# Kernel optimization log

Hardware: AMD Instinct MI355X
Metric: run time of the kernel (lower is better)

The kernel has to match this reference:

```python
import jax, jax.numpy as jnp
import numpy as np

N = 100000        # nodes
E = 1600000       # edges (avg degree 16)
IN_C = 128
HID = 128
OUT_C = 18


def setup_inputs() -> dict:
    key = jax.random.key(0)
    k_x, k_e, k_w1, k_b1, k_w2, k_b2 = jax.random.split(key, 6)
    x = jax.random.normal(k_x, (N, IN_C), dtype=jnp.float32)
    edge_index = jax.random.randint(k_e, (2, E), 0, N, dtype=jnp.int64)
    # Glorot-ish init for linear weights, zero bias (PyG GCNConv defaults)
    W1 = jax.random.normal(k_w1, (IN_C, HID), dtype=jnp.float32) / np.sqrt(IN_C)
    b1 = jnp.zeros((HID,), dtype=jnp.float32)
    W2 = jax.random.normal(k_w2, (HID, OUT_C), dtype=jnp.float32) / np.sqrt(HID)
    b2 = jnp.zeros((OUT_C,), dtype=jnp.float32)
    return {"x": x, "edge_index": edge_index, "W1": W1, "b1": b1, "W2": W2, "b2": b2}


def _gcn_conv(x, src, dst, norm, W, b, n_nodes):
    # PyG GCNConv: linear transform, then normalized scatter-add aggregation
    h = x @ W                                   # [N, d_out]
    msg = h[src] * norm[:, None]                # gather + scale: [E+N, d_out]
    out = jax.ops.segment_sum(msg, dst, num_segments=n_nodes)
    return out + b


def reference(x, edge_index, W1, b1, W2, b2):
    src, dst = edge_index[0], edge_index[1]
    loop = jnp.arange(N, dtype=edge_index.dtype)
    src_f = jnp.concatenate([src, loop])        # add self-loops
    dst_f = jnp.concatenate([dst, loop])
    # symmetric normalization deg^-1/2[src] * deg^-1/2[dst] (with self-loops)
    deg = jax.ops.segment_sum(jnp.ones_like(dst_f, dtype=x.dtype), dst_f, num_segments=N)
    dinv = jnp.where(deg > 0, jax.lax.rsqrt(deg), 0.0)
    norm = dinv[src_f] * dinv[dst_f]            # [E+N]

    h = _gcn_conv(x, src_f, dst_f, norm, W1, b1, N)
    h = jax.nn.relu(h)
    # dropout is identity in eval mode (training=False)
    h = _gcn_conv(h, src_f, dst_f, norm, W2, b2, N)
    return jax.nn.log_softmax(h, axis=1)
```

## Files before the change

kernel.cpp:

```cpp
#include <hip/hip_runtime.h>
#include <math.h>

#define NN 100000
#define NE 1600000
#define CH  128
#define CO  18
#define NPB 256
#define NBUK ((NN + NPB - 1) / NPB)
#define EPB 4096
#define NBB ((NE + EPB - 1) / EPB)

typedef unsigned int uint;
typedef unsigned short ushort;
typedef float floatx4 __attribute__((ext_vector_type(4)));
typedef short short8 __attribute__((ext_vector_type(8)));
typedef ushort ushort4v __attribute__((ext_vector_type(4)));

__device__ __forceinline__ float bf_lo(uint u) { return __uint_as_float(u << 16); }
__device__ __forceinline__ float bf_hi(uint u) { return __uint_as_float(u & 0xFFFF0000u); }
__device__ __forceinline__ ushort f2bf(float f) {
    uint u = __float_as_uint(f);
    u += 0x7FFFu + ((u >> 16) & 1u);
    return (ushort)(u >> 16);
}
__device__ __forceinline__ uint pack_bf16(float a, float b) {
    return (uint)f2bf(a) | ((uint)f2bf(b) << 16);
}


__global__ __launch_bounds__(256) void k_bhist(const int* __restrict__ dst,
                                               int* __restrict__ bcnt) {
    __shared__ int h[NBUK];
    int tid = threadIdx.x;
    for (int i = tid; i < NBUK; i += 256) h[i] = 0;
    __syncthreads();
    int e0 = blockIdx.x * EPB;
#pragma unroll
    for (int i = 0; i < EPB / 256; ++i) {
        int e = e0 + i * 256 + tid;
        if (e < NE) atomicAdd(&h[dst[e] >> 8], 1);
    }
    __syncthreads();
    for (int i = tid; i < NBUK; i += 256)
        if (h[i]) atomicAdd(&bcnt[i], h[i]);
}

__global__ __launch_bounds__(512) void k_bscan(const int* __restrict__ bcnt,
                                               int* __restrict__ bbase,
                                               int* __restrict__ bcur) {
    __shared__ int s[512];
    int tid = threadIdx.x;
    int c = (tid < NBUK) ? bcnt[tid] : 0;
    s[tid] = c;
    __syncthreads();
    for (int off = 1; off < 512; off <<= 1) {
        int t = (tid >= off) ? s[tid - off] : 0;
        __syncthreads();
        s[tid] += t;
        __syncthreads();
    }
    if (tid < NBUK) {
        int ex = s[tid] - c;
        bbase[tid] = ex;
        bcur[tid] = ex;
    }
    if (tid == NBUK) bbase[NBUK] = NE;
}

__global__ __launch_bounds__(256) void k_bin(const int* __restrict__ src,
                                             const int* __restrict__ dst,
                                             int* __restrict__ bcur,
                                             uint* __restrict__ etmp) {
    __shared__ int h[NBUK];
    __shared__ int base[NBUK];
    int tid = threadIdx.x;
    for (int i = tid; i < NBUK; i += 256) h[i] = 0;
    __syncthreads();

    int e0 = blockIdx.x * EPB;
    int sv[EPB / 256], dv[EPB / 256];
#pragma unroll
    for (int i = 0; i < EPB / 256; ++i) {
        int e = e0 + i * 256 + tid;
        if (e < NE) {
            sv[i] = src[e];
            dv[i] = dst[e];
            atomicAdd(&h[dv[i] >> 8], 1);
        } else {
            dv[i] = -1;
        }
    }
    __syncthreads();
    for (int i = tid; i < NBUK; i += 256)
        base[i] = h[i] ? atomicAdd(&bcur[i], h[i]) : 0;
    __syncthreads();
    for (int i = tid; i < NBUK; i += 256) h[i] = 0;
    __syncthreads();
#pragma unroll
    for (int i = 0; i < EPB / 256; ++i) {
        if (dv[i] >= 0) {
            int b = dv[i] >> 8;
            int pos = base[b] + atomicAdd(&h[b], 1);
            etmp[pos] = ((uint)sv[i] << 8) | ((uint)dv[i] & 255u);
        }
    }
}

__global__ __launch_bounds__(256) void k_pass2(const int* __restrict__ bbase,
                                               const uint* __restrict__ etmp,
                                               int* __restrict__ row_start,
                                               float* __restrict__ dinv,
                                               int* __restrict__ csr_src) {
    __shared__ int hist[NPB];
    __shared__ int s[NPB];
    __shared__ int cur[NPB];
    int tid = threadIdx.x;
    int b = blockIdx.x;
    int e0 = bbase[b], e1 = bbase[b + 1];

    hist[tid] = 0;
    __syncthreads();
    for (int e = e0 + tid; e < e1; e += 256)
        atomicAdd(&hist[etmp[e] & 255u], 1);
    __syncthreads();

    int c = hist[tid];
    s[tid] = c;
    __syncthreads();
    for (int off = 1; off < 256; off <<= 1) {
        int t = (tid >= off) ? s[tid - off] : 0;
        __syncthreads();
        s[tid] += t;
        __syncthreads();
    }
    int pfx = s[tid] - c;
    s[tid] = pfx;
    cur[tid] = 0;

    int node = b * NPB + tid;
    if (node < NN) {
        row_start[node] = e0 + pfx;
        dinv[node] = rsqrtf((float)c + 1.0f);
    }
    if (b == NBUK - 1 && tid == 0) row_start[NN] = NE;
    __syncthreads();

    for (int e = e0 + tid; e < e1; e += 256) {
        uint r = etmp[e];
        int n = (int)(r & 255u);
        int p = e0 + s[n] + atomicAdd(&cur[n], 1);
        csr_src[p] = (int)(r >> 8);
    }
}


__global__ __launch_bounds__(256) void k_wprep(const float* __restrict__ W1,
                                               ushort* __restrict__ Wt) {
    int t = blockIdx.x * 256 + threadIdx.x;
    if (t < 128 * 128) {
        int k = t >> 7, n = t & 127;
        Wt[n * 128 + k] = f2bf(W1[t]);
    }
}


__global__ __launch_bounds__(256, 2) void k_gemm1(const float* __restrict__ x,
                                                  const uint* __restrict__ Wtg,
                                                  ushort* __restrict__ h1s) {
    __shared__ ushort As[128 * 128];
    __shared__ ushort Bs[128 * 128];
    int tid = threadIdx.x;
    int row0 = blockIdx.x * 128;

    for (int i = 0; i < 32; ++i) {
        int j = i * 256 + tid;
        int n = j >> 6, ku = j & 63;
        int uidx = (n * 64 + ku) ^ ((n & 7) << 2);
        ((uint*)Bs)[uidx] = Wtg[j];
    }
    for (int i = 0; i < 16; ++i) {
        int flat = i * 256 + tid;
        int r = flat >> 5, c4 = flat & 31;
        int gr = row0 + r;
        float4 v = (gr < NN) ? ((const float4*)x)[(size_t)gr * 32 + c4]
                             : make_float4(0.f, 0.f, 0.f, 0.f);
        ushort4v p;
        p.x = f2bf(v.x); p.y = f2bf(v.y); p.z = f2bf(v.z); p.w = f2bf(v.w);
        int idx = (r * 128 + c4 * 4) ^ ((r & 7) << 3);
        *(ushort4v*)&As[idx] = p;
    }
    __syncthreads();

    int lane = tid & 63;
    int wave = tid >> 6;
    int wrow = wave * 32;
    int lr = lane & 15;
    int lk8 = (lane >> 4) * 8;

    floatx4 acc[2][8];
#pragma unroll
    for (int a = 0; a < 2; ++a)
#pragma unroll
        for (int b = 0; b < 8; ++b) acc[a][b] = (floatx4)(0.0f);

#pragma unroll
    for (int ks = 0; ks < 4; ++ks) {
        int k0 = ks * 32 + lk8;
        int r0r = wrow + lr;
        int r1r = wrow + 16 + lr;
        short8 a0 = *(const short8*)&As[(r0r * 128 + k0) ^ ((r0r & 7) << 3)];
        short8 a1 = *(const short8*)&As[(r1r * 128 + k0) ^ ((r1r & 7) << 3)];
#pragma unroll
        for (int nt = 0; nt < 8; ++nt) {
            int n = nt * 16 + lr;
            short8 bf = *(const short8*)&Bs[(n * 128 + k0) ^ ((n & 7) << 3)];
            acc[0][nt] = __builtin_amdgcn_mfma_f32_16x16x32_bf16(a0, bf, acc[0][nt], 0, 0, 0);
            acc[1][nt] = __builtin_amdgcn_mfma_f32_16x16x32_bf16(a1, bf, acc[1][nt], 0, 0, 0);
        }
    }

    int drow = (lane >> 4) * 4;
#pragma unroll
    for (int rt = 0; rt < 2; ++rt) {
#pragma unroll
        for (int i = 0; i < 4; ++i) {
            int gr = row0 + wrow + rt * 16 + drow + i;
            if (gr < NN) {
                size_t base = (size_t)gr * 128;
#pragma unroll
                for (int nt = 0; nt < 8; ++nt)
                    h1s[base + nt * 16 + lr] = f2bf(acc[rt][nt][i]);
            }
        }
    }
}


__global__ __launch_bounds__(256) void k_agg1(const int* __restrict__ row_start,
                                              const int* __restrict__ csr_src,
                                              const float* __restrict__ dinv,
                                              const uint* __restrict__ h1u,
                                              const float* __restrict__ b1,
                                              uint* __restrict__ h1ru) {
    int wave = threadIdx.x >> 6;
    int lane = threadIdx.x & 63;
    int i = blockIdx.x * 4 + wave;
    if (i >= NN) return;
    int r0 = row_start[i], r1 = row_start[i + 1];
    float di = dinv[i];
    float ax = 0.0f, ay = 0.0f;

    int j = r0;
    for (; j + 7 < r1; j += 8) {
        int s0 = csr_src[j],     s1 = csr_src[j + 1];
        int s2 = csr_src[j + 2], s3 = csr_src[j + 3];
        int s4 = csr_src[j + 4], s5 = csr_src[j + 5];
        int s6 = csr_src[j + 6], s7 = csr_src[j + 7];
        float w0 = dinv[s0] * di, w1 = dinv[s1] * di;
        float w2 = dinv[s2] * di, w3 = dinv[s3] * di;
        float w4 = dinv[s4] * di, w5 = dinv[s5] * di;
        float w6 = dinv[s6] * di, w7 = dinv[s7] * di;
        uint u0 = h1u[(size_t)s0 * 64 + lane];
        uint u1 = h1u[(size_t)s1 * 64 + lane];
        uint u2 = h1u[(size_t)s2 * 64 + lane];
        uint u3 = h1u[(size_t)s3 * 64 + lane];
        uint u4 = h1u[(size_t)s4 * 64 + lane];
        uint u5 = h1u[(size_t)s5 * 64 + lane];
        uint u6 = h1u[(size_t)s6 * 64 + lane];
        uint u7 = h1u[(size_t)s7 * 64 + lane];
        ax += w0 * bf_lo(u0) + w1 * bf_lo(u1) + w2 * bf_lo(u2) + w3 * bf_lo(u3)
            + w4 * bf_lo(u4) + w5 * bf_lo(u5) + w6 * bf_lo(u6) + w7 * bf_lo(u7);
        ay += w0 * bf_hi(u0) + w1 * bf_hi(u1) + w2 * bf_hi(u2) + w3 * bf_hi(u3)
            + w4 * bf_hi(u4) + w5 * bf_hi(u5) + w6 * bf_hi(u6) + w7 * bf_hi(u7);
    }
    for (; j < r1; ++j) {
        int s0 = csr_src[j];
        float w0 = dinv[s0] * di;
        uint u0 = h1u[(size_t)s0 * 64 + lane];
        ax += w0 * bf_lo(u0);
        ay += w0 * bf_hi(u0);
    }

    uint us = h1u[(size_t)i * 64 + lane];
    float2 bb = ((const float2*)b1)[lane];
    float di2 = di * di;
    float ox = fmaxf(ax + di2 * bf_lo(us) + bb.x, 0.0f);
    float oy = fmaxf(ay + di2 * bf_hi(us) + bb.y, 0.0f);
    h1ru[(size_t)i * 64 + lane] = pack_bf16(ox, oy);
}


__global__ __launch_bounds__(256, 2) void k_gemm2(const uint* __restrict__ h1ru,
                                                  const float* __restrict__ W2,
                                                  ushort* __restrict__ h2b) {
    __shared__ float xs[128][129];
    __shared__ float Ws[128 * 18];
    int row0 = blockIdx.x * 128;
    int tid = threadIdx.x;

    for (int i = tid; i < 128 * 18; i += 256) Ws[i] = W2[i];
    for (int i = tid; i < 128 * 64; i += 256) {
        int r = i >> 6, c2 = i & 63;
        int gr = row0 + r;
        uint u = (gr < NN) ? h1ru[(size_t)gr * 64 + c2] : 0u;
        xs[r][2 * c2]     = bf_lo(u);
        xs[r][2 * c2 + 1] = bf_hi(u);
    }
    __syncthreads();

    int rl   = tid & 127;
    int half = tid >> 7;
    int j0   = half * 9;
    float acc[9];
#pragma unroll
    for (int j = 0; j < 9; ++j) acc[j] = 0.0f;

#pragma unroll 4
    for (int k = 0; k < 128; ++k) {
        float xv = xs[rl][k];
#pragma unroll
        for (int j = 0; j < 9; ++j)
            acc[j] += xv * Ws[k * 18 + j0 + j];
    }
    int gr = row0 + rl;
    if (gr < NN) {
#pragma unroll
        for (int j = 0; j < 9; ++j)
            h2b[(size_t)gr * 24 + j0 + j] = f2bf(acc[j]);
    }
}


__device__ __forceinline__ void acc_row(float* acc, float w,
                                        uint4 a, uint4 b, uint c) {
    acc[0]  += w * bf_lo(a.x); acc[1]  += w * bf_hi(a.x);
    acc[2]  += w * bf_lo(a.y); acc[3]  += w * bf_hi(a.y);
    acc[4]  += w * bf_lo(a.z); acc[5]  += w * bf_hi(a.z);
    acc[6]  += w * bf_lo(a.w); acc[7]  += w * bf_hi(a.w);
    acc[8]  += w * bf_lo(b.x); acc[9]  += w * bf_hi(b.x);
    acc[10] += w * bf_lo(b.y); acc[11] += w * bf_hi(b.y);
    acc[12] += w * bf_lo(b.z); acc[13] += w * bf_hi(b.z);
    acc[14] += w * bf_lo(b.w); acc[15] += w * bf_hi(b.w);
    acc[16] += w * bf_lo(c);   acc[17] += w * bf_hi(c);
}

__global__ __launch_bounds__(256) void k_agg2(const int* __restrict__ row_start,
                                              const int* __restrict__ csr_src,
                                              const float* __restrict__ dinv,
                                              const uint* __restrict__ h2u,
                                              const float* __restrict__ b2,
                                              float* __restrict__ out) {
    int i = blockIdx.x * 256 + threadIdx.x;
    if (i >= NN) return;
    int r0 = row_start[i], r1 = row_start[i + 1];
    float di = dinv[i];
    float acc[CO];
#pragma unroll
    for (int j = 0; j < CO; ++j) acc[j] = 0.0f;

    int e = r0;
    for (; e + 3 < r1; e += 4) {
        int s0 = csr_src[e],     s1 = csr_src[e + 1];
        int s2 = csr_src[e + 2], s3 = csr_src[e + 3];
        float w0 = dinv[s0] * di, w1 = dinv[s1] * di;
        float w2 = dinv[s2] * di, w3 = dinv[s3] * di;
        const uint4* p0 = (const uint4*)(h2u + (size_t)s0 * 12);
        const uint4* p1 = (const uint4*)(h2u + (size_t)s1 * 12);
        const uint4* p2 = (const uint4*)(h2u + (size_t)s2 * 12);
        const uint4* p3 = (const uint4*)(h2u + (size_t)s3 * 12);
        uint4 a0 = p0[0], b0 = p0[1]; uint c0 = ((const uint*)p0)[8];
        uint4 a1 = p1[0], b1v = p1[1]; uint c1 = ((const uint*)p1)[8];
        uint4 a2 = p2[0], b2v = p2[1]; uint c2 = ((const uint*)p2)[8];
        uint4 a3 = p3[0], b3v = p3[1]; uint c3 = ((const uint*)p3)[8];
        acc_row(acc, w0, a0, b0, c0);
        acc_row(acc, w1, a1, b1v, c1);
        acc_row(acc, w2, a2, b2v, c2);
        acc_row(acc, w3, a3, b3v, c3);
    }
    for (; e < r1; ++e) {
        int s = csr_src[e];
        float w = dinv[s] * di;
        const uint4* p = (const uint4*)(h2u + (size_t)s * 12);
        uint4 a = p[0], b = p[1]; uint c = ((const uint*)p)[8];
        acc_row(acc, w, a, b, c);
    }

    float di2 = di * di;
    const uint4* pi = (const uint4*)(h2u + (size_t)i * 12);
    uint4 ia = pi[0], ib = pi[1]; uint ic = ((const uint*)pi)[8];
    acc_row(acc, di2, ia, ib, ic);

    float m = -1e30f;
#pragma unroll
    for (int j = 0; j < CO; ++j) {
        acc[j] += b2[j];
        m = fmaxf(m, acc[j]);
    }
    float sum = 0.0f;
#pragma unroll
    for (int j = 0; j < CO; ++j) sum += expf(acc[j] - m);
    float lse = logf(sum);
    float* op = out + (size_t)i * CO;
#pragma unroll
    for (int j = 0; j < CO; ++j) op[j] = acc[j] - m - lse;
}


extern "C" void kernel_launch(void* const* d_in, const int* in_sizes, int n_in,
                              void* d_out, int out_size, void* d_ws, size_t ws_size,
                              hipStream_t stream) {
    const float* x  = (const float*)d_in[0];
    const int*   ei = (const int*)d_in[1];
    const float* W1 = (const float*)d_in[2];
    const float* b1 = (const float*)d_in[3];
    const float* W2 = (const float*)d_in[4];
    const float* b2 = (const float*)d_in[5];
    float* out = (float*)d_out;

    const int* src = ei;
    const int* dst = ei + NE;

    uint* h1u  = (uint*)d_ws;
    uint* h1ru = h1u + (size_t)NN * 64;
    uint* h2u  = h1ru + (size_t)NN * 64;
    float* dinv = (float*)(h2u + (size_t)NN * 12);
    int* row_start = (int*)(dinv + NN);
    int* csr_src   = row_start + NN + 1;
    uint* etmp     = (uint*)(csr_src + NE);
    int* bcnt      = (int*)(etmp + NE);
    int* bbase     = bcnt + NBUK;
    int* bcur      = bbase + NBUK + 1;
    ushort* Wt     = (ushort*)(bcur + NBUK);

    hipMemsetAsync(bcnt, 0, NBUK * sizeof(int), stream);

    k_bhist<<<NBB, 256, 0, stream>>>(dst, bcnt);
    k_bscan<<<1, 512, 0, stream>>>(bcnt, bbase, bcur);
    k_bin<<<NBB, 256, 0, stream>>>(src, dst, bcur, etmp);
    k_pass2<<<NBUK, 256, 0, stream>>>(bbase, etmp, row_start, dinv, csr_src);

    k_wprep<<<64, 256, 0, stream>>>(W1, Wt);
    k_gemm1<<<(NN + 127) / 128, 256, 0, stream>>>(x, (const uint*)Wt, (ushort*)h1u);
    k_agg1<<<(NN + 3) / 4, 256, 0, stream>>>(row_start, csr_src, dinv, h1u, b1, h1ru);
    k_gemm2<<<(NN + 127) / 128, 256, 0, stream>>>(h1ru, W2, (ushort*)h2u);
    k_agg2<<<(NN + 255) / 256, 256, 0, stream>>>(row_start, csr_src, dinv, h2u, b2, out);
}
```

Baseline: 247.0 us.

## Fuse histogram with GEMM1, split agg2 across thread pairs, shrink agg1 blocks

The dst-histogram kernel and the first GEMM now run as one launch, with blocks branching on their index and sharing LDS through a union. W1 is converted to bf16 inside each GEMM block, so the separate weight-prep kernel and its launch go away. agg2 now gives each node to two threads that each handle 12 padded channels and combine the softmax max and sum with a lane shuffle, which doubles parallelism. gemm2 zero-fills the padding columns so the upper half reads defined values. agg1 uses 128-thread blocks, and every GEMM block now redoes the W1 conversion with strided global reads.

```diff
diff --git a/kernel.cpp b/kernel.cpp
--- a/kernel.cpp
+++ b/kernel.cpp
@@ -28,22 +28,99 @@
 }
 
 
-__global__ __launch_bounds__(256) void k_bhist(const int* __restrict__ dst,
-                                               int* __restrict__ bcnt) {
-    __shared__ int h[NBUK];
+union FatLDS {
+    int h[NBUK];
+    struct { ushort As[128 * 128]; ushort Bs[128 * 128]; } g;
+};
+
+__global__ __launch_bounds__(256, 2) void k_fat1(const int* __restrict__ dst,
+                                                 int* __restrict__ bcnt,
+                                                 const float* __restrict__ x,
+                                                 const float* __restrict__ W1,
+                                                 ushort* __restrict__ h1s) {
+    __shared__ FatLDS L;
     int tid = threadIdx.x;
-    for (int i = tid; i < NBUK; i += 256) h[i] = 0;
-    __syncthreads();
-    int e0 = blockIdx.x * EPB;
-#pragma unroll
-    for (int i = 0; i < EPB / 256; ++i) {
-        int e = e0 + i * 256 + tid;
-        if (e < NE) atomicAdd(&h[dst[e] >> 8], 1);
-    }
-    __syncthreads();
-    for (int i = tid; i < NBUK; i += 256)
-        if (h[i]) atomicAdd(&bcnt[i], h[i]);
-}
+
+    if (blockIdx.x < NBB) {
+        for (int i = tid; i < NBUK; i += 256) L.h[i] = 0;
+        __syncthreads();
+        int e0 = blockIdx.x * EPB;
+#pragma unroll
+        for (int i = 0; i < EPB / 256; ++i) {
+            int e = e0 + i * 256 + tid;
+            if (e < NE) atomicAdd(&L.h[dst[e] >> 8], 1);
+        }
+        __syncthreads();
+        for (int i = tid; i < NBUK; i += 256)
+            if (L.h[i]) atomicAdd(&bcnt[i], L.h[i]);
+        return;
+    }
+
+    int row0 = (blockIdx.x - NBB) * 128;
+
+    for (int p = tid; p < 8192; p += 256) {
+        int kp = p >> 7, n = p & 127;
+        float w0 = W1[(2 * kp) * 128 + n];
+        float w1 = W1[(2 * kp + 1) * 128 + n];
+        ((uint*)L.g.Bs)[(n * 64 + kp) ^ ((n & 7) << 2)] = pack_bf16(w0, w1);
+    }
+    for (int i = 0; i < 16; ++i) {
+        int flat = i * 256 + tid;
+        int r = flat >> 5, c4 = flat & 31;
+        int gr = row0 + r;
+        float4 v = (gr < NN) ? ((const float4*)x)[(size_t)gr * 32 + c4]
+                             : make_float4(0.f, 0.f, 0.f, 0.f);
+        ushort4v p;
+        p.x = f2bf(v.x); p.y = f2bf(v.y); p.z = f2bf(v.z); p.w = f2bf(v.w);
+        int idx = (r * 128 + c4 * 4) ^ ((r & 7) << 3);
+        *(ushort4v*)&L.g.As[idx] = p;
+    }
+    __syncthreads();
+
+    int lane = tid & 63;
+    int wave = tid >> 6;
+    int wrow = wave * 32;
+    int lr = lane & 15;
+    int lk8 = (lane >> 4) * 8;
+
+    floatx4 acc[2][8];
+#pragma unroll
+    for (int a = 0; a < 2; ++a)
+#pragma unroll
+        for (int b = 0; b < 8; ++b) acc[a][b] = (floatx4)(0.0f);
+
+#pragma unroll
+    for (int ks = 0; ks < 4; ++ks) {
+        int k0 = ks * 32 + lk8;
+        int r0r = wrow + lr;
+        int r1r = wrow + 16 + lr;
+        short8 a0 = *(const short8*)&L.g.As[(r0r * 128 + k0) ^ ((r0r & 7) << 3)];
+        short8 a1 = *(const short8*)&L.g.As[(r1r * 128 + k0) ^ ((r1r & 7) << 3)];
+#pragma unroll
+        for (int nt = 0; nt < 8; ++nt) {
+            int n = nt * 16 + lr;
+            short8 bf = *(const short8*)&L.g.Bs[(n * 128 + k0) ^ ((n & 7) << 3)];
+            acc[0][nt] = __builtin_amdgcn_mfma_f32_16x16x32_bf16(a0, bf, acc[0][nt], 0, 0, 0);
+            acc[1][nt] = __builtin_amdgcn_mfma_f32_16x16x32_bf16(a1, bf, acc[1][nt], 0, 0, 0);
+        }
+    }
+
+    int drow = (lane >> 4) * 4;
+#pragma unroll
+    for (int rt = 0; rt < 2; ++rt) {
+#pragma unroll
+        for (int i = 0; i < 4; ++i) {
+            int gr = row0 + wrow + rt * 16 + drow + i;
+            if (gr < NN) {
+                size_t base = (size_t)gr * 128;
+#pragma unroll
+                for (int nt = 0; nt < 8; ++nt)
+                    h1s[base + nt * 16 + lr] = f2bf(acc[rt][nt][i]);
+            }
+        }
+    }
+}
+
 
 __global__ __launch_bounds__(512) void k_bscan(const int* __restrict__ bcnt,
                                                int* __restrict__ bbase,
@@ -154,89 +231,7 @@
 }
 
 
-__global__ __launch_bounds__(256) void k_wprep(const float* __restrict__ W1,
-                                               ushort* __restrict__ Wt) {
-    int t = blockIdx.x * 256 + threadIdx.x;
-    if (t < 128 * 128) {
-        int k = t >> 7, n = t & 127;
-        Wt[n * 128 + k] = f2bf(W1[t]);
-    }
-}
-
-
-__global__ __launch_bounds__(256, 2) void k_gemm1(const float* __restrict__ x,
-                                                  const uint* __restrict__ Wtg,
-                                                  ushort* __restrict__ h1s) {
-    __shared__ ushort As[128 * 128];
-    __shared__ ushort Bs[128 * 128];
-    int tid = threadIdx.x;
-    int row0 = blockIdx.x * 128;
-
-    for (int i = 0; i < 32; ++i) {
-        int j = i * 256 + tid;
-        int n = j >> 6, ku = j & 63;
-        int uidx = (n * 64 + ku) ^ ((n & 7) << 2);
-        ((uint*)Bs)[uidx] = Wtg[j];
-    }
-    for (int i = 0; i < 16; ++i) {
-        int flat = i * 256 + tid;
-        int r = flat >> 5, c4 = flat & 31;
-        int gr = row0 + r;
-        float4 v = (gr < NN) ? ((const float4*)x)[(size_t)gr * 32 + c4]
-                             : make_float4(0.f, 0.f, 0.f, 0.f);
-        ushort4v p;
-        p.x = f2bf(v.x); p.y = f2bf(v.y); p.z = f2bf(v.z); p.w = f2bf(v.w);
-        int idx = (r * 128 + c4 * 4) ^ ((r & 7) << 3);
-        *(ushort4v*)&As[idx] = p;
-    }
-    __syncthreads();
-
-    int lane = tid & 63;
-    int wave = tid >> 6;
-    int wrow = wave * 32;
-    int lr = lane & 15;
-    int lk8 = (lane >> 4) * 8;
-
-    floatx4 acc[2][8];
-#pragma unroll
-    for (int a = 0; a < 2; ++a)
-#pragma unroll
-        for (int b = 0; b < 8; ++b) acc[a][b] = (floatx4)(0.0f);
-
-#pragma unroll
-    for (int ks = 0; ks < 4; ++ks) {
-        int k0 = ks * 32 + lk8;
-        int r0r = wrow + lr;
-        int r1r = wrow + 16 + lr;
-        short8 a0 = *(const short8*)&As[(r0r * 128 + k0) ^ ((r0r & 7) << 3)];
-        short8 a1 = *(const short8*)&As[(r1r * 128 + k0) ^ ((r1r & 7) << 3)];
-#pragma unroll
-        for (int nt = 0; nt < 8; ++nt) {
-            int n = nt * 16 + lr;
-            short8 bf = *(const short8*)&Bs[(n * 128 + k0) ^ ((n & 7) << 3)];
-            acc[0][nt] = __builtin_amdgcn_mfma_f32_16x16x32_bf16(a0, bf, acc[0][nt], 0, 0, 0);
-            acc[1][nt] = __builtin_amdgcn_mfma_f32_16x16x32_bf16(a1, bf, acc[1][nt], 0, 0, 0);
-        }
-    }
-
-    int drow = (lane >> 4) * 4;
-#pragma unroll
-    for (int rt = 0; rt < 2; ++rt) {
-#pragma unroll
-        for (int i = 0; i < 4; ++i) {
-            int gr = row0 + wrow + rt * 16 + drow + i;
-            if (gr < NN) {
-                size_t base = (size_t)gr * 128;
-#pragma unroll
-                for (int nt = 0; nt < 8; ++nt)
-                    h1s[base + nt * 16 + lr] = f2bf(acc[rt][nt][i]);
-            }
-        }
-    }
-}
-
-
-__global__ __launch_bounds__(256) void k_agg1(const int* __restrict__ row_start,
+__global__ __launch_bounds__(128) void k_agg1(const int* __restrict__ row_start,
                                               const int* __restrict__ csr_src,
                                               const float* __restrict__ dinv,
                                               const uint* __restrict__ h1u,
@@ -244,7 +239,7 @@
                                               uint* __restrict__ h1ru) {
     int wave = threadIdx.x >> 6;
     int lane = threadIdx.x & 63;
-    int i = blockIdx.x * 4 + wave;
+    int i = blockIdx.x * 2 + wave;
     if (i >= NN) return;
     int r0 = row_start[i], r1 = row_start[i + 1];
     float di = dinv[i];
@@ -327,21 +322,22 @@
 #pragma unroll
         for (int j = 0; j < 9; ++j)
             h2b[(size_t)gr * 24 + j0 + j] = f2bf(acc[j]);
-    }
-}
-
-
-__device__ __forceinline__ void acc_row(float* acc, float w,
-                                        uint4 a, uint4 b, uint c) {
-    acc[0]  += w * bf_lo(a.x); acc[1]  += w * bf_hi(a.x);
-    acc[2]  += w * bf_lo(a.y); acc[3]  += w * bf_hi(a.y);
-    acc[4]  += w * bf_lo(a.z); acc[5]  += w * bf_hi(a.z);
-    acc[6]  += w * bf_lo(a.w); acc[7]  += w * bf_hi(a.w);
-    acc[8]  += w * bf_lo(b.x); acc[9]  += w * bf_hi(b.x);
-    acc[10] += w * bf_lo(b.y); acc[11] += w * bf_hi(b.y);
-    acc[12] += w * bf_lo(b.z); acc[13] += w * bf_hi(b.z);
-    acc[14] += w * bf_lo(b.w); acc[15] += w * bf_hi(b.w);
-    acc[16] += w * bf_lo(c);   acc[17] += w * bf_hi(c);
+        if (half) {
+#pragma unroll
+            for (int j = 0; j < 6; ++j)
+                h2b[(size_t)gr * 24 + 18 + j] = 0;
+        }
+    }
+}
+
+
+__device__ __forceinline__ void acc6(float* acc, float wgt, uint4 av, uint2 cv) {
+    acc[0]  += wgt * bf_lo(av.x); acc[1]  += wgt * bf_hi(av.x);
+    acc[2]  += wgt * bf_lo(av.y); acc[3]  += wgt * bf_hi(av.y);
+    acc[4]  += wgt * bf_lo(av.z); acc[5]  += wgt * bf_hi(av.z);
+    acc[6]  += wgt * bf_lo(av.w); acc[7]  += wgt * bf_hi(av.w);
+    acc[8]  += wgt * bf_lo(cv.x); acc[9]  += wgt * bf_hi(cv.x);
+    acc[10] += wgt * bf_lo(cv.y); acc[11] += wgt * bf_hi(cv.y);
 }
 
 __global__ __launch_bounds__(256) void k_agg2(const int* __restrict__ row_start,
@@ -350,13 +346,16 @@
                                               const uint* __restrict__ h2u,
                                               const float* __restrict__ b2,
                                               float* __restrict__ out) {
-    int i = blockIdx.x * 256 + threadIdx.x;
+    int t = blockIdx.x * 256 + threadIdx.x;
+    int i = t >> 1;
+    int half = t & 1;
     if (i >= NN) return;
     int r0 = row_start[i], r1 = row_start[i + 1];
     float di = dinv[i];
-    float acc[CO];
-#pragma unroll
-    for (int j = 0; j < CO; ++j) acc[j] = 0.0f;
+    int base = half * 6;
+    float acc[12];
+#pragma unroll
+    for (int j = 0; j < 12; ++j) acc[j] = 0.0f;
 
     int e = r0;
     for (; e + 3 < r1; e += 4) {
@@ -364,45 +363,57 @@
         int s2 = csr_src[e + 2], s3 = csr_src[e + 3];
         float w0 = dinv[s0] * di, w1 = dinv[s1] * di;
         float w2 = dinv[s2] * di, w3 = dinv[s3] * di;
-        const uint4* p0 = (const uint4*)(h2u + (size_t)s0 * 12);
-        const uint4* p1 = (const uint4*)(h2u + (size_t)s1 * 12);
-        const uint4* p2 = (const uint4*)(h2u + (size_t)s2 * 12);
-        const uint4* p3 = (const uint4*)(h2u + (size_t)s3 * 12);
-        uint4 a0 = p0[0], b0 = p0[1]; uint c0 = ((const uint*)p0)[8];
-        uint4 a1 = p1[0], b1v = p1[1]; uint c1 = ((const uint*)p1)[8];
-        uint4 a2 = p2[0], b2v = p2[1]; uint c2 = ((const uint*)p2)[8];
-        uint4 a3 = p3[0], b3v = p3[1]; uint c3 = ((const uint*)p3)[8];
-        acc_row(acc, w0, a0, b0, c0);
-        acc_row(acc, w1, a1, b1v, c1);
-        acc_row(acc, w2, a2, b2v, c2);
-        acc_row(acc, w3, a3, b3v, c3);
+        const uint* p0 = h2u + (size_t)s0 * 12 + base;
+        const uint* p1 = h2u + (size_t)s1 * 12 + base;
+        const uint* p2 = h2u + (size_t)s2 * 12 + base;
+        const uint* p3 = h2u + (size_t)s3 * 12 + base;
+        uint4 a0 = *(const uint4*)p0; uint2 c0 = *(const uint2*)(p0 + 4);
+        uint4 a1 = *(const uint4*)p1; uint2 c1 = *(const uint2*)(p1 + 4);
+        uint4 a2 = *(const uint4*)p2; uint2 c2 = *(const uint2*)(p2 + 4);
+        uint4 a3 = *(const uint4*)p3; uint2 c3 = *(const uint2*)(p3 + 4);
+        acc6(acc, w0, a0, c0);
+        acc6(acc, w1, a1, c1);
+        acc6(acc, w2, a2, c2);
+        acc6(acc, w3, a3, c3);
     }
     for (; e < r1; ++e) {
         int s = csr_src[e];
         float w = dinv[s] * di;
-        const uint4* p = (const uint4*)(h2u + (size_t)s * 12);
-        uint4 a = p[0], b = p[1]; uint c = ((const uint*)p)[8];
-        acc_row(acc, w, a, b, c);
+        const uint* p = h2u + (size_t)s * 12 + base;
+        uint4 a = *(const uint4*)p; uint2 c = *(const uint2*)(p + 4);
+        acc6(acc, w, a, c);
     }
 
     float di2 = di * di;
-    const uint4* pi = (const uint4*)(h2u + (size_t)i * 12);
-    uint4 ia = pi[0], ib = pi[1]; uint ic = ((const uint*)pi)[8];
-    acc_row(acc, di2, ia, ib, ic);
-
+    const uint* pi = h2u + (size_t)i * 12 + base;
+    uint4 ia = *(const uint4*)pi; uint2 ic = *(const uint2*)(pi + 4);
+    acc6(acc, di2, ia, ic);
+
+    int ch0 = half * 12;
     float m = -1e30f;
 #pragma unroll
-    for (int j = 0; j < CO; ++j) {
-        acc[j] += b2[j];
-        m = fmaxf(m, acc[j]);
-    }
+    for (int j = 0; j < 12; ++j) {
+        int ch = ch0 + j;
+        if (ch < CO) {
+            acc[j] += b2[ch];
+            m = fmaxf(m, acc[j]);
+        }
+    }
+    m = fmaxf(m, __shfl_xor(m, 1));
     float sum = 0.0f;
 #pragma unroll
-    for (int j = 0; j < CO; ++j) sum += expf(acc[j] - m);
+    for (int j = 0; j < 12; ++j) {
+        int ch = ch0 + j;
+        if (ch < CO) sum += expf(acc[j] - m);
+    }
+    sum += __shfl_xor(sum, 1);
     float lse = logf(sum);
     float* op = out + (size_t)i * CO;
 #pragma unroll
-    for (int j = 0; j < CO; ++j) op[j] = acc[j] - m - lse;
+    for (int j = 0; j < 12; ++j) {
+        int ch = ch0 + j;
+        if (ch < CO) op[ch] = acc[j] - m - lse;
+    }
 }
 
 
@@ -430,18 +441,15 @@
     int* bcnt      = (int*)(etmp + NE);
     int* bbase     = bcnt + NBUK;
     int* bcur      = bbase + NBUK + 1;
-    ushort* Wt     = (ushort*)(bcur + NBUK);
 
     hipMemsetAsync(bcnt, 0, NBUK * sizeof(int), stream);
 
-    k_bhist<<<NBB, 256, 0, stream>>>(dst, bcnt);
+    k_fat1<<<NBB + (NN + 127) / 128, 256, 0, stream>>>(dst, bcnt, x, W1, (ushort*)h1u);
     k_bscan<<<1, 512, 0, stream>>>(bcnt, bbase, bcur);
     k_bin<<<NBB, 256, 0, stream>>>(src, dst, bcur, etmp);
     k_pass2<<<NBUK, 256, 0, stream>>>(bbase, etmp, row_start, dinv, csr_src);
 
-    k_wprep<<<64, 256, 0, stream>>>(W1, Wt);
-    k_gemm1<<<(NN + 127) / 128, 256, 0, stream>>>(x, (const uint*)Wt, (ushort*)h1u);
-    k_agg1<<<(NN + 3) / 4, 256, 0, stream>>>(row_start, csr_src, dinv, h1u, b1, h1ru);
+    k_agg1<<<(NN + 1) / 2, 128, 0, stream>>>(row_start, csr_src, dinv, h1u, b1, h1ru);
     k_gemm2<<<(NN + 127) / 128, 256, 0, stream>>>(h1ru, W2, (ushort*)h2u);
-    k_agg2<<<(NN + 255) / 256, 256, 0, stream>>>(row_start, csr_src, dinv, h2u, b2, out);
-}
+    k_agg2<<<(2 * NN + 255) / 256, 256, 0, stream>>>(row_start, csr_src, dinv, h2u, b2, out);
+}
```

After: 255.4 us. 1.03x slower.
